# Optimization experiments

Measured on AMD Instinct MI355X. Metric: run time of the kernel, lower is better.

The kernel has to match this reference:

```python
import jax, jax.numpy as jnp
import numpy as np

B, C, D_IN, D_H, D_QK = 64, 512, 1024, 1024, 512
EPS = 1e-5


def setup_inputs() -> dict:
    key = jax.random.key(0)
    ks = jax.random.split(key, 24)
    din2 = D_IN + D_H  # concat([x, h]) feature dim
    s_qk = 1.0 / np.sqrt(din2)
    inp = {
        "x": jax.random.normal(ks[0], (B, C, D_IN), jnp.float32),
        "h": jax.random.normal(ks[1], (B, C, D_H), jnp.float32),
    }
    i = 2
    for g in ("r", "z", "n"):
        inp[f"Wq_{g}"] = jax.random.normal(ks[i], (din2, D_QK), jnp.float32) * s_qk; i += 1
        inp[f"bq_{g}"] = jnp.zeros((D_QK,), jnp.float32)
        inp[f"Wk_{g}"] = jax.random.normal(ks[i], (din2, D_QK), jnp.float32) * s_qk; i += 1
        inp[f"bk_{g}"] = jnp.zeros((D_QK,), jnp.float32)
        inp[f"Wv_{g}"] = jax.random.normal(ks[i], (din2, D_H), jnp.float32) * s_qk; i += 1
        inp[f"bv_{g}"] = jnp.zeros((D_H,), jnp.float32)
    inp["gamma"] = jnp.ones((D_H,), jnp.float32)
    inp["beta"] = jnp.zeros((D_H,), jnp.float32)
    return inp


def _self_attention(xin, Wq, bq, Wk, bk, Wv, bv):
    # xin: (B, C, 2D) ; attention over channel axis C
    Q = xin @ Wq + bq            # (B, C, d_qk)
    K = xin @ Wk + bk            # (B, C, d_qk)
    V = xin @ Wv + bv            # (B, C, d_h)
    scale = 1.0 / jnp.sqrt(jnp.asarray(Q.shape[-1], jnp.float32))
    scores = jnp.einsum("bcd,bed->bce", Q, K) * scale   # (B, C, C)
    attn = jax.nn.softmax(scores, axis=-1)
    return jnp.einsum("bce,bed->bcd", attn, V)          # (B, C, d_h)


def reference(x, h,
              Wq_r, bq_r, Wk_r, bk_r, Wv_r, bv_r,
              Wq_z, bq_z, Wk_z, bk_z, Wv_z, bv_z,
              Wq_n, bq_n, Wk_n, bk_n, Wv_n, bv_n,
              gamma, beta):
    xh = jnp.concatenate([x, h], axis=2)
    r = _self_attention(xh, Wq_r, bq_r, Wk_r, bk_r, Wv_r, bv_r)
    z = _self_attention(xh, Wq_z, bq_z, Wk_z, bk_z, Wv_z, bv_z)
    reset = jax.nn.sigmoid(r)
    update = jax.nn.sigmoid(z)
    xhr = jnp.concatenate([x, h * reset], axis=2)
    n = _self_attention(xhr, Wq_n, bq_n, Wk_n, bk_n, Wv_n, bv_n)
    new_state = (1.0 - update) * h + update * jnp.tanh(n)
    # LayerNorm over last dim
    mu = jnp.mean(new_state, axis=-1, keepdims=True)
    var = jnp.var(new_state, axis=-1, keepdims=True)
    return (new_state - mu) * jax.lax.rsqrt(var + EPS) * gamma + beta
```

## Files before the change

kernel.cpp:

```cpp
#include <hip/hip_runtime.h>
#include <math.h>

typedef __attribute__((ext_vector_type(8))) short short8;
typedef __attribute__((ext_vector_type(4))) float f32x4;

#define EPI_BF16   0
#define EPI_SCORES 1
#define EPI_R      2
#define EPI_Z      3
#define EPI_N      4

__device__ __forceinline__ unsigned short f2bf(float f) {
    unsigned int u = __float_as_uint(f);
    u += 0x7fffu + ((u >> 16) & 1u);
    return (unsigned short)(u >> 16);
}
__device__ __forceinline__ float bf2f(unsigned short s) {
    return __uint_as_float(((unsigned int)s) << 16);
}

struct alignas(8) us4 { unsigned short a, b, c, d; };

#define GLD_LDS16(gp, lp) \
    __builtin_amdgcn_global_load_lds((const __attribute__((address_space(1))) unsigned int*)(gp), \
                                     (__attribute__((address_space(3))) unsigned int*)(lp), 16, 0, 0)

__device__ __forceinline__ void BARF() {
    asm volatile("" ::: "memory");
    __builtin_amdgcn_s_barrier();
    asm volatile("" ::: "memory");
}
#define LGKM0 asm volatile("s_waitcnt lgkmcnt(0)" ::: "memory")

template<int EPI, int SWZ>
__global__ void __launch_bounds__(512, 2)
gemm256(const unsigned short* __restrict__ A, long long sAb, int lda,
        const unsigned short* __restrict__ Bt, long long sBb, int ldb,
        const float* __restrict__ bias,
        void* __restrict__ C, long long sCb, int ldc,
        int K, float scale,
        const float* __restrict__ hptr,
        const unsigned short* __restrict__ updptr)
{
    extern __shared__ char smem[];

    const int z = blockIdx.z;
    A  += (size_t)z * (size_t)sAb;
    Bt += (size_t)z * (size_t)sBb;

    int bx, by;
    if (SWZ) {
        const int bid = blockIdx.y * 8 + blockIdx.x;
        const int xcd = bid & 7, i = bid >> 3;
        bx = i & 7;
        by = (xcd << 4) | (i >> 3);
    } else {
        bx = blockIdx.x; by = blockIdx.y;
    }
    const int m0 = by * 256;
    const int n0 = bx * 256;

    const int tid = threadIdx.x;
    const int w  = tid >> 6;
    const int l  = tid & 63;
    const int wr = w >> 2;
    const int wc = w & 3;
    const int lr = l & 15;
    const int lg = l >> 4;
    const int rs = (lr & 7) << 4;

    const int srw = l >> 3;
    const int scb = ((l & 7) << 4) ^ (srw << 4);
    const int ldsw = w << 10;

    const long long ldab = (long long)lda * 2;
    const long long ldbb = (long long)ldb * 2;

    f32x4 acc[2][4][4] = {};
    short8 a[4][2], b[4][2];

#define STAGE_A(kt, buf) { \
    const char* g_ = (const char*)A + (size_t)(m0 + w*8 + srw) * ldab + (size_t)(kt)*2 + scb; \
    char* d_ = smem + (buf)*65536 + ldsw; \
    _Pragma("unroll") \
    for (int j = 0; j < 4; ++j) \
        GLD_LDS16(g_ + (size_t)(j*64) * ldab, d_ + j*8192); }

#define STAGE_B(kt, buf) { \
    const char* g_ = (const char*)Bt + (size_t)(n0 + w*8 + srw) * ldbb + (size_t)(kt)*2 + scb; \
    char* d_ = smem + (buf)*65536 + 32768 + ldsw; \
    _Pragma("unroll") \
    for (int j = 0; j < 4; ++j) \
        GLD_LDS16(g_ + (size_t)(j*64) * ldbb, d_ + j*8192); }

#define LDA8(MH, buf) { \
    const char* Ab_ = smem + (buf)*65536; \
    _Pragma("unroll") \
    for (int mf = 0; mf < 4; ++mf) { \
        const int row_ = wr*128 + (MH)*64 + mf*16 + lr; \
        _Pragma("unroll") \
        for (int kk = 0; kk < 2; ++kk) \
            a[mf][kk] = *(const short8*)(Ab_ + row_*128 + ((kk*64 + lg*16) ^ rs)); } }

#define LDB4(BH, buf) { \
    const char* Bb_ = smem + (buf)*65536 + 32768; \
    _Pragma("unroll") \
    for (int nf = 0; nf < 2; ++nf) { \
        const int row_ = wc*64 + (BH)*32 + nf*16 + lr; \
        _Pragma("unroll") \
        for (int kk = 0; kk < 2; ++kk) \
            b[(BH)*2+nf][kk] = *(const short8*)(Bb_ + row_*128 + ((kk*64 + lg*16) ^ rs)); } }

#define MMA16(MH, BH) { \
    __builtin_amdgcn_s_setprio(1); \
    _Pragma("unroll") \
    for (int kk = 0; kk < 2; ++kk) \
    _Pragma("unroll") \
    for (int mf = 0; mf < 4; ++mf) \
    _Pragma("unroll") \
    for (int nf = 0; nf < 2; ++nf) \
        acc[MH][mf][(BH)*2+nf] = __builtin_amdgcn_mfma_f32_16x16x32_bf16( \
            a[mf][kk], b[(BH)*2+nf][kk], acc[MH][mf][(BH)*2+nf], 0, 0, 0); \
    __builtin_amdgcn_s_setprio(0); }

    STAGE_A(0, 0); STAGE_B(0, 0);
    STAGE_A(64, 1); STAGE_B(64, 1);
    asm volatile("s_waitcnt vmcnt(8)" ::: "memory");
    BARF();

    const int NT = K >> 6;
    for (int t = 0; t < NT; ++t) {
        const int p = t & 1;
        LDA8(0, p); LDB4(0, p);
        BARF(); LGKM0;
        MMA16(0, 0);
        BARF();
        LDB4(1, p);
        BARF(); LGKM0;
        MMA16(0, 1);
        BARF();
        LDA8(1, p);
        BARF(); LGKM0;
        MMA16(1, 1);
        BARF();
        if (t + 2 < NT) {
            STAGE_A((t + 2) * 64, p); STAGE_B((t + 2) * 64, p);
            asm volatile("s_waitcnt vmcnt(8)" ::: "memory");
        } else {
            asm volatile("s_waitcnt vmcnt(0)" ::: "memory");
        }
        BARF();
        MMA16(1, 0);
        BARF();
    }

    const int Mb = gridDim.y << 8;
    const size_t zc = (size_t)z * (size_t)sCb;
    #pragma unroll
    for (int mh = 0; mh < 2; ++mh) {
        #pragma unroll
        for (int mf = 0; mf < 4; ++mf) {
            #pragma unroll
            for (int nf = 0; nf < 4; ++nf) {
                const int col = n0 + wc * 64 + nf * 16 + lr;
                const float bval = (EPI == EPI_BF16) ? bias[col] : 0.0f;
                #pragma unroll
                for (int r = 0; r < 4; ++r) {
                    const int row = m0 + wr * 128 + mh * 64 + mf * 16 + lg * 4 + r;
                    float v = acc[mh][mf][nf][r] + bval;
                    if (EPI == EPI_BF16) {
                        ((unsigned short*)C)[zc + (size_t)row * ldc + col] = f2bf(v);
                    } else if (EPI == EPI_SCORES) {
                        ((float*)C)[zc + (size_t)row * ldc + col] = v * scale;
                    } else if (EPI == EPI_R) {
                        const size_t flat = (size_t)z * Mb + row;
                        const float hh = hptr[flat * 1024 + col];
                        const float sg = 1.0f / (1.0f + __expf(-v));
                        ((unsigned short*)C)[flat * 2048 + 1024 + col] = f2bf(hh * sg);
                    } else if (EPI == EPI_Z) {
                        const size_t flat = (size_t)z * Mb + row;
                        const float sg = 1.0f / (1.0f + __expf(-v));
                        ((unsigned short*)C)[flat * 1024 + col] = f2bf(sg);
                    } else {
                        const size_t flat = (size_t)z * Mb + row;
                        const float u  = bf2f(updptr[flat * 1024 + col]);
                        const float hh = hptr[flat * 1024 + col];
                        ((float*)C)[flat * 1024 + col] = (1.0f - u) * hh + u * tanhf(v);
                    }
                }
            }
        }
    }
#undef STAGE_A
#undef STAGE_B
#undef LDA8
#undef LDB4
#undef MMA16
}


__global__ void __launch_bounds__(256)
prep_xh(const float* __restrict__ x, const float* __restrict__ h, unsigned short* __restrict__ xh)
{
    const size_t t = (size_t)blockIdx.x * 256 + threadIdx.x;
    const size_t f = t * 4;
    const size_t row = f >> 10, col = f & 1023;
    const float4 vx = *(const float4*)(x + f);
    const float4 vh = *(const float4*)(h + f);
    us4 ox = { f2bf(vx.x), f2bf(vx.y), f2bf(vx.z), f2bf(vx.w) };
    us4 oh = { f2bf(vh.x), f2bf(vh.y), f2bf(vh.z), f2bf(vh.w) };
    *(us4*)(xh + row * 2048 + col)        = ox;
    *(us4*)(xh + row * 2048 + 1024 + col) = oh;
}

__global__ void __launch_bounds__(256)
transpose_w(const float* __restrict__ W, unsigned short* __restrict__ WT, int N)
{
    __shared__ float t[32][33];
    const int k0 = blockIdx.y * 32, n0 = blockIdx.x * 32;
    const int tx = threadIdx.x & 31, ty = threadIdx.x >> 5;
    #pragma unroll
    for (int i = 0; i < 4; ++i)
        t[ty + i * 8][tx] = W[(size_t)(k0 + ty + i * 8) * N + n0 + tx];
    __syncthreads();
    #pragma unroll
    for (int i = 0; i < 4; ++i)
        WT[(size_t)(n0 + ty + i * 8) * 2048 + k0 + tx] = f2bf(t[tx][ty + i * 8]);
}

__global__ void __launch_bounds__(256)
transpose_v(const unsigned short* __restrict__ V, unsigned short* __restrict__ Vt)
{
    __shared__ unsigned short t[32][34];
    const int z = blockIdx.z;
    const unsigned short* in = V + (size_t)z * 512 * 2048;
    unsigned short* outp = Vt + (size_t)z * 1024 * 512;
    const int c0 = blockIdx.x * 32, r0 = blockIdx.y * 32;
    const int tx = threadIdx.x & 31, ty = threadIdx.x >> 5;
    #pragma unroll
    for (int i = 0; i < 4; ++i)
        t[ty + i * 8][tx] = in[(size_t)(r0 + ty + i * 8) * 2048 + c0 + tx];
    __syncthreads();
    #pragma unroll
    for (int i = 0; i < 4; ++i)
        outp[(size_t)(c0 + ty + i * 8) * 512 + r0 + tx] = t[tx][ty + i * 8];
}

__global__ void __launch_bounds__(256)
softmax512(const float* __restrict__ S, unsigned short* __restrict__ P)
{
    const int row = blockIdx.x * 4 + (threadIdx.x >> 6);
    const int l = threadIdx.x & 63;
    const float* s = S + (size_t)row * 512;
    const float4 v0 = ((const float4*)s)[l];
    const float4 v1 = ((const float4*)s)[64 + l];
    float m = fmaxf(fmaxf(fmaxf(v0.x, v0.y), fmaxf(v0.z, v0.w)),
                    fmaxf(fmaxf(v1.x, v1.y), fmaxf(v1.z, v1.w)));
    #pragma unroll
    for (int d = 32; d; d >>= 1) m = fmaxf(m, __shfl_xor(m, d));
    float e0 = __expf(v0.x - m), e1 = __expf(v0.y - m), e2 = __expf(v0.z - m), e3 = __expf(v0.w - m);
    float e4 = __expf(v1.x - m), e5 = __expf(v1.y - m), e6 = __expf(v1.z - m), e7 = __expf(v1.w - m);
    float sum = e0 + e1 + e2 + e3 + e4 + e5 + e6 + e7;
    #pragma unroll
    for (int d = 32; d; d >>= 1) sum += __shfl_xor(sum, d);
    const float inv = 1.0f / sum;
    unsigned short* p = P + (size_t)row * 512;
    us4 aa = { f2bf(e0 * inv), f2bf(e1 * inv), f2bf(e2 * inv), f2bf(e3 * inv) };
    us4 bb = { f2bf(e4 * inv), f2bf(e5 * inv), f2bf(e6 * inv), f2bf(e7 * inv) };
    ((us4*)p)[l] = aa;
    ((us4*)p)[64 + l] = bb;
}

__global__ void __launch_bounds__(256)
layernorm1024(float* __restrict__ Y, const float* __restrict__ gamma, const float* __restrict__ beta)
{
    const int row = blockIdx.x * 4 + (threadIdx.x >> 6);
    const int l = threadIdx.x & 63;
    float* p = Y + (size_t)row * 1024;
    float4 v[4];
    float s = 0.0f, s2 = 0.0f;
    #pragma unroll
    for (int i = 0; i < 4; ++i) {
        v[i] = ((const float4*)p)[i * 64 + l];
        s  += v[i].x + v[i].y + v[i].z + v[i].w;
        s2 += v[i].x * v[i].x + v[i].y * v[i].y + v[i].z * v[i].z + v[i].w * v[i].w;
    }
    #pragma unroll
    for (int d = 32; d; d >>= 1) { s += __shfl_xor(s, d); s2 += __shfl_xor(s2, d); }
    const float mu = s * (1.0f / 1024.0f);
    const float var = s2 * (1.0f / 1024.0f) - mu * mu;
    const float inv = rsqrtf(var + 1e-5f);
    #pragma unroll
    for (int i = 0; i < 4; ++i) {
        const float4 gv = ((const float4*)gamma)[i * 64 + l];
        const float4 bv = ((const float4*)beta)[i * 64 + l];
        float4 o;
        o.x = (v[i].x - mu) * inv * gv.x + bv.x;
        o.y = (v[i].y - mu) * inv * gv.y + bv.y;
        o.z = (v[i].z - mu) * inv * gv.z + bv.z;
        o.w = (v[i].w - mu) * inv * gv.w + bv.w;
        ((float4*)p)[i * 64 + l] = o;
    }
}

__global__ void __launch_bounds__(256)
concat_bias(const float* __restrict__ a, const float* __restrict__ b,
            const float* __restrict__ c, float* __restrict__ o)
{
    const int i = blockIdx.x * 256 + threadIdx.x;
    o[i] = (i < 512) ? a[i] : (i < 1024) ? b[i - 512] : c[i - 1024];
}

extern "C" void kernel_launch(void* const* d_in, const int* in_sizes, int n_in,
                              void* d_out, int out_size, void* d_ws, size_t ws_size,
                              hipStream_t stream)
{
    (void)in_sizes; (void)n_in; (void)out_size; (void)ws_size;

    const float* x = (const float*)d_in[0];
    const float* h = (const float*)d_in[1];
    const float* Wf[9]; const float* bia[9];
    for (int g = 0; g < 3; ++g)
        for (int j = 0; j < 3; ++j) {
            Wf[g * 3 + j]  = (const float*)d_in[2 + g * 6 + j * 2];
            bia[g * 3 + j] = (const float*)d_in[2 + g * 6 + j * 2 + 1];
        }
    const float* gamma = (const float*)d_in[20];
    const float* beta  = (const float*)d_in[21];
    float* out = (float*)d_out;

    const int LDS_BYTES = 131072;
    hipFuncSetAttribute((const void*)gemm256<EPI_BF16, 1>,   hipFuncAttributeMaxDynamicSharedMemorySize, LDS_BYTES);
    hipFuncSetAttribute((const void*)gemm256<EPI_SCORES, 0>, hipFuncAttributeMaxDynamicSharedMemorySize, LDS_BYTES);
    hipFuncSetAttribute((const void*)gemm256<EPI_R, 0>,      hipFuncAttributeMaxDynamicSharedMemorySize, LDS_BYTES);
    hipFuncSetAttribute((const void*)gemm256<EPI_Z, 0>,      hipFuncAttributeMaxDynamicSharedMemorySize, LDS_BYTES);
    hipFuncSetAttribute((const void*)gemm256<EPI_N, 0>,      hipFuncAttributeMaxDynamicSharedMemorySize, LDS_BYTES);

    char* ws = (char*)d_ws;
    size_t off = 0;
    auto alloc = [&](size_t bytes) -> void* {
        void* p = ws + off; off += (bytes + 255) & ~(size_t)255; return p;
    };
    unsigned short* xh  = (unsigned short*)alloc((size_t)32768 * 2048 * 2);
    unsigned short* WT  = (unsigned short*)alloc((size_t)12582912 * 2);
    unsigned short* QKV = (unsigned short*)alloc((size_t)32768 * 2048 * 2);
    unsigned short* Vt  = (unsigned short*)alloc((size_t)32768 * 1024 * 2);
    float*          Sc  = (float*)alloc((size_t)64 * 512 * 512 * 4);
    unsigned short* Pb  = (unsigned short*)alloc((size_t)64 * 512 * 512 * 2);
    unsigned short* upd = (unsigned short*)alloc((size_t)32768 * 1024 * 2);
    float*          bct = (float*)alloc((size_t)3 * 2048 * 4);

    size_t wtoff[9];
    {
        size_t o = 0;
        for (int g = 0; g < 3; ++g) {
            wtoff[g * 3 + 0] = o; o += (size_t)512 * 2048;
            wtoff[g * 3 + 1] = o; o += (size_t)512 * 2048;
            wtoff[g * 3 + 2] = o; o += (size_t)1024 * 2048;
        }
    }

    prep_xh<<<32768, 256, 0, stream>>>(x, h, xh);
    for (int i = 0; i < 9; ++i) {
        const int N = (i % 3 == 2) ? 1024 : 512;
        transpose_w<<<dim3(N / 32, 64, 1), 256, 0, stream>>>(Wf[i], WT + wtoff[i], N);
    }
    for (int g = 0; g < 3; ++g)
        concat_bias<<<8, 256, 0, stream>>>(bia[g * 3 + 0], bia[g * 3 + 1], bia[g * 3 + 2], bct + g * 2048);

    const float scscale = 0.044194173824159216f;

    auto gate = [&](int g, int epi) {
        const unsigned short* wT = WT + wtoff[g * 3 + 0];
        gemm256<EPI_BF16, 1><<<dim3(8, 128, 1), 512, LDS_BYTES, stream>>>(
            xh, 0, 2048, wT, 0, 2048, bct + g * 2048, QKV, 0, 2048, 2048, 0.0f, nullptr, nullptr);
        transpose_v<<<dim3(32, 16, 64), 256, 0, stream>>>(QKV + 1024, Vt);
        gemm256<EPI_SCORES, 0><<<dim3(2, 2, 64), 512, LDS_BYTES, stream>>>(
            QKV, 1048576, 2048, QKV + 512, 1048576, 2048, nullptr,
            Sc, 262144, 512, 512, scscale, nullptr, nullptr);
        softmax512<<<8192, 256, 0, stream>>>(Sc, Pb);
        if (epi == EPI_Z)
            gemm256<EPI_Z, 0><<<dim3(4, 2, 64), 512, LDS_BYTES, stream>>>(
                Pb, 262144, 512, Vt, 524288, 512, nullptr, upd, 0, 1024, 512, 0.0f, nullptr, nullptr);
        else if (epi == EPI_R)
            gemm256<EPI_R, 0><<<dim3(4, 2, 64), 512, LDS_BYTES, stream>>>(
                Pb, 262144, 512, Vt, 524288, 512, nullptr, xh, 0, 2048, 512, 0.0f, h, nullptr);
        else
            gemm256<EPI_N, 0><<<dim3(4, 2, 64), 512, LDS_BYTES, stream>>>(
                Pb, 262144, 512, Vt, 524288, 512, nullptr, out, 0, 1024, 512, 0.0f, h, upd);
    };

    gate(1, EPI_Z);
    gate(0, EPI_R);
    gate(2, EPI_N);
    layernorm1024<<<8192, 256, 0, stream>>>(out, gamma, beta);
}
```

Measured before the change: 1.575 ms.

## Restructure GEMM main loop into half-tile staged pipeline with fewer barriers

Splits each 256-row A/B LDS tile into two 128-row halves and interleaves the global-to-LDS loads of individual halves with the MFMA phases. The loop is unrolled over two k-steps with a peeled tail. It uses vmcnt(4) waits and drops the extra barriers between fragment reads and MFMAs, so loads should overlap better with compute. Each wave now holds all 8 A fragments, which raises register pressure, and the finer-grained reuse of LDS regions depends on the barrier ordering being correct.

```diff
diff --git a/kernel.cpp b/kernel.cpp
--- a/kernel.cpp
+++ b/kernel.cpp
@@ -25,12 +25,11 @@
     __builtin_amdgcn_global_load_lds((const __attribute__((address_space(1))) unsigned int*)(gp), \
                                      (__attribute__((address_space(3))) unsigned int*)(lp), 16, 0, 0)
 
-__device__ __forceinline__ void BARF() {
-    asm volatile("" ::: "memory");
-    __builtin_amdgcn_s_barrier();
-    asm volatile("" ::: "memory");
-}
-#define LGKM0 asm volatile("s_waitcnt lgkmcnt(0)" ::: "memory")
+#define BAR    __builtin_amdgcn_s_barrier()
+#define LGKM0  do { asm volatile("s_waitcnt lgkmcnt(0)" ::: "memory"); \
+                    __builtin_amdgcn_sched_barrier(0); } while (0)
+#define VMC4   asm volatile("s_waitcnt vmcnt(4)" ::: "memory")
+#define VMC0   asm volatile("s_waitcnt vmcnt(0)" ::: "memory")
 
 template<int EPI, int SWZ>
 __global__ void __launch_bounds__(512, 2)
@@ -71,42 +70,37 @@
 
     const int srw = l >> 3;
     const int scb = ((l & 7) << 4) ^ (srw << 4);
-    const int ldsw = w << 10;
 
     const long long ldab = (long long)lda * 2;
     const long long ldbb = (long long)ldb * 2;
 
     f32x4 acc[2][4][4] = {};
-    short8 a[4][2], b[4][2];
-
-#define STAGE_A(kt, buf) { \
-    const char* g_ = (const char*)A + (size_t)(m0 + w*8 + srw) * ldab + (size_t)(kt)*2 + scb; \
-    char* d_ = smem + (buf)*65536 + ldsw; \
-    _Pragma("unroll") \
-    for (int j = 0; j < 4; ++j) \
-        GLD_LDS16(g_ + (size_t)(j*64) * ldab, d_ + j*8192); }
-
-#define STAGE_B(kt, buf) { \
-    const char* g_ = (const char*)Bt + (size_t)(n0 + w*8 + srw) * ldbb + (size_t)(kt)*2 + scb; \
-    char* d_ = smem + (buf)*65536 + 32768 + ldsw; \
-    _Pragma("unroll") \
-    for (int j = 0; j < 4; ++j) \
-        GLD_LDS16(g_ + (size_t)(j*64) * ldbb, d_ + j*8192); }
+    short8 a[8][2], b[4][2];
+
+#define AR(buf, half) (smem + (buf)*65536 + (half)*16384)
+#define BR(buf, half) (smem + (buf)*65536 + 32768 + (half)*16384)
+
+#define STAGE_H(gbase, ldbytes, r0abs, kt, region) { \
+    _Pragma("unroll") \
+    for (int j = 0; j < 2; ++j) { \
+        const char* g_ = (const char*)(gbase) + \
+            (size_t)((r0abs) + j*64 + w*8 + srw) * (ldbytes) + (size_t)(kt)*2 + scb; \
+        GLD_LDS16(g_, (region) + j*8192 + (w<<10)); } }
 
 #define LDA8(MH, buf) { \
-    const char* Ab_ = smem + (buf)*65536; \
+    const char* Ab_ = AR(buf, wr); \
     _Pragma("unroll") \
     for (int mf = 0; mf < 4; ++mf) { \
-        const int row_ = wr*128 + (MH)*64 + mf*16 + lr; \
+        const int row_ = (MH)*64 + mf*16 + lr; \
         _Pragma("unroll") \
         for (int kk = 0; kk < 2; ++kk) \
-            a[mf][kk] = *(const short8*)(Ab_ + row_*128 + ((kk*64 + lg*16) ^ rs)); } }
+            a[(MH)*4+mf][kk] = *(const short8*)(Ab_ + row_*128 + ((kk*64 + lg*16) ^ rs)); } }
 
 #define LDB4(BH, buf) { \
-    const char* Bb_ = smem + (buf)*65536 + 32768; \
+    const char* Bb_ = BR(buf, wc >> 1); \
     _Pragma("unroll") \
     for (int nf = 0; nf < 2; ++nf) { \
-        const int row_ = wc*64 + (BH)*32 + nf*16 + lr; \
+        const int row_ = (wc&1)*64 + (BH)*32 + nf*16 + lr; \
         _Pragma("unroll") \
         for (int kk = 0; kk < 2; ++kk) \
             b[(BH)*2+nf][kk] = *(const short8*)(Bb_ + row_*128 + ((kk*64 + lg*16) ^ rs)); } }
@@ -120,38 +114,64 @@
     _Pragma("unroll") \
     for (int nf = 0; nf < 2; ++nf) \
         acc[MH][mf][(BH)*2+nf] = __builtin_amdgcn_mfma_f32_16x16x32_bf16( \
-            a[mf][kk], b[(BH)*2+nf][kk], acc[MH][mf][(BH)*2+nf], 0, 0, 0); \
+            a[(MH)*4+mf][kk], b[(BH)*2+nf][kk], acc[MH][mf][(BH)*2+nf], 0, 0, 0); \
     __builtin_amdgcn_s_setprio(0); }
 
-    STAGE_A(0, 0); STAGE_B(0, 0);
-    STAGE_A(64, 1); STAGE_B(64, 1);
-    asm volatile("s_waitcnt vmcnt(8)" ::: "memory");
-    BARF();
-
-    const int NT = K >> 6;
-    for (int t = 0; t < NT; ++t) {
-        const int p = t & 1;
-        LDA8(0, p); LDB4(0, p);
-        BARF(); LGKM0;
-        MMA16(0, 0);
-        BARF();
-        LDB4(1, p);
-        BARF(); LGKM0;
-        MMA16(0, 1);
-        BARF();
-        LDA8(1, p);
-        BARF(); LGKM0;
+    STAGE_H(A,  ldab, m0 + 0,   0,  AR(0,0));
+    STAGE_H(A,  ldab, m0 + 128, 0,  AR(0,1));
+    STAGE_H(Bt, ldbb, n0 + 0,   0,  BR(0,0));
+    STAGE_H(Bt, ldbb, n0 + 128, 0,  BR(0,1));
+    STAGE_H(A,  ldab, m0 + 0,   64, AR(1,0));
+    STAGE_H(A,  ldab, m0 + 128, 64, AR(1,1));
+
+    const int NIT = K >> 7;
+    for (int it = 0; it < NIT - 1; ++it) {
+        const int kt0 = it << 7;
+        VMC4; BAR;
+        STAGE_H(Bt, ldbb, n0 + 0,   kt0 + 64,  BR(1,0));
+        LDA8(0, 0); LDB4(0, 0);
+        LGKM0; MMA16(0, 0);
+        BAR;
+        STAGE_H(Bt, ldbb, n0 + 128, kt0 + 64,  BR(1,1));
+        LDA8(1, 0); LDB4(1, 0);
+        LGKM0; MMA16(0, 1);
+        BAR;
+        STAGE_H(A,  ldab, m0 + 0,   kt0 + 128, AR(0,0));
         MMA16(1, 1);
-        BARF();
-        if (t + 2 < NT) {
-            STAGE_A((t + 2) * 64, p); STAGE_B((t + 2) * 64, p);
-            asm volatile("s_waitcnt vmcnt(8)" ::: "memory");
-        } else {
-            asm volatile("s_waitcnt vmcnt(0)" ::: "memory");
-        }
-        BARF();
+        BAR;
+        STAGE_H(A,  ldab, m0 + 128, kt0 + 128, AR(0,1));
         MMA16(1, 0);
-        BARF();
+        VMC4; BAR;
+        STAGE_H(Bt, ldbb, n0 + 0,   kt0 + 128, BR(0,0));
+        LDA8(0, 1); LDB4(0, 1);
+        LGKM0; MMA16(0, 0);
+        BAR;
+        STAGE_H(Bt, ldbb, n0 + 128, kt0 + 128, BR(0,1));
+        LDA8(1, 1); LDB4(1, 1);
+        LGKM0; MMA16(0, 1);
+        BAR;
+        STAGE_H(A,  ldab, m0 + 0,   kt0 + 192, AR(1,0));
+        MMA16(1, 1);
+        BAR;
+        STAGE_H(A,  ldab, m0 + 128, kt0 + 192, AR(1,1));
+        MMA16(1, 0);
+    }
+    {
+        const int kt0 = (NIT - 1) << 7;
+        VMC4; BAR;
+        STAGE_H(Bt, ldbb, n0 + 0,   kt0 + 64, BR(1,0));
+        LDA8(0, 0); LDB4(0, 0); LGKM0; MMA16(0, 0);
+        BAR;
+        STAGE_H(Bt, ldbb, n0 + 128, kt0 + 64, BR(1,1));
+        LDA8(1, 0); LDB4(1, 0); LGKM0; MMA16(0, 1);
+        BAR; MMA16(1, 1);
+        BAR; MMA16(1, 0);
+        VMC0; BAR;
+        LDA8(0, 1); LDB4(0, 1); LGKM0; MMA16(0, 0);
+        BAR;
+        LDA8(1, 1); LDB4(1, 1); LGKM0; MMA16(0, 1);
+        BAR; MMA16(1, 1);
+        BAR; MMA16(1, 0);
     }
 
     const int Mb = gridDim.y << 8;
@@ -191,8 +211,9 @@
             }
         }
     }
-#undef STAGE_A
-#undef STAGE_B
+#undef AR
+#undef BR
+#undef STAGE_H
 #undef LDA8
 #undef LDB4
 #undef MMA16
```

Result: slower. 1.978 ms (+25.6%).

## Interleave split global-to-LDS staging with MFMA phases and drop barriers

Applied to the files above, without the earlier changes.

Prefetching in the GEMM main loop is split into quarter-tile global_load_lds chunks, issued between the LDS fragment reads and the MFMA phases instead of all at once before the last phase. B is now prefetched one tile ahead into the alternate buffer, while A stays two tiles ahead in the current buffer. Several barriers and the explicit lgkmcnt(0) waits are removed, and the vmcnt waits are retuned to the new load order. The aim is to overlap global loads with matrix work and cut synchronisation stalls. The cost is a more fragile ordering of LDS reads against in-flight overwrites.

```diff
diff --git a/kernel.cpp b/kernel.cpp
--- a/kernel.cpp
+++ b/kernel.cpp
@@ -25,12 +25,10 @@
     __builtin_amdgcn_global_load_lds((const __attribute__((address_space(1))) unsigned int*)(gp), \
                                      (__attribute__((address_space(3))) unsigned int*)(lp), 16, 0, 0)
 
-__device__ __forceinline__ void BARF() {
-    asm volatile("" ::: "memory");
-    __builtin_amdgcn_s_barrier();
-    asm volatile("" ::: "memory");
-}
-#define LGKM0 asm volatile("s_waitcnt lgkmcnt(0)" ::: "memory")
+#define BAR   do { asm volatile("" ::: "memory"); __builtin_amdgcn_s_barrier(); \
+                   asm volatile("" ::: "memory"); } while (0)
+#define VMC4  asm volatile("s_waitcnt vmcnt(4)" ::: "memory")
+#define VMC0  asm volatile("s_waitcnt vmcnt(0)" ::: "memory")
 
 template<int EPI, int SWZ>
 __global__ void __launch_bounds__(512, 2)
@@ -71,7 +69,6 @@
 
     const int srw = l >> 3;
     const int scb = ((l & 7) << 4) ^ (srw << 4);
-    const int ldsw = w << 10;
 
     const long long ldab = (long long)lda * 2;
     const long long ldbb = (long long)ldb * 2;
@@ -79,22 +76,25 @@
     f32x4 acc[2][4][4] = {};
     short8 a[4][2], b[4][2];
 
-#define STAGE_A(kt, buf) { \
-    const char* g_ = (const char*)A + (size_t)(m0 + w*8 + srw) * ldab + (size_t)(kt)*2 + scb; \
-    char* d_ = smem + (buf)*65536 + ldsw; \
-    _Pragma("unroll") \
-    for (int j = 0; j < 4; ++j) \
-        GLD_LDS16(g_ + (size_t)(j*64) * ldab, d_ + j*8192); }
-
-#define STAGE_B(kt, buf) { \
-    const char* g_ = (const char*)Bt + (size_t)(n0 + w*8 + srw) * ldbb + (size_t)(kt)*2 + scb; \
-    char* d_ = smem + (buf)*65536 + 32768 + ldsw; \
-    _Pragma("unroll") \
-    for (int j = 0; j < 4; ++j) \
-        GLD_LDS16(g_ + (size_t)(j*64) * ldbb, d_ + j*8192); }
+#define STAGE1(gbase, ldbytes, grow0, ldsoff) { \
+    const char* g_ = (const char*)(gbase) + \
+        (size_t)((grow0) + w*8 + srw) * (ldbytes) + scb; \
+    GLD_LDS16(g_, smem + (ldsoff) + (w << 10)); }
+
+#define AOFF(buf) ((buf)*65536)
+#define BOFF(buf) ((buf)*65536 + 32768)
+
+#define STAGE_A0(kt, buf) { STAGE1(A, ldab, m0 + 0   + 0*0, AOFF(buf) + 0);      \
+                            STAGE1(A + (size_t)(kt)*0, ldab, m0 + 128, AOFF(buf) + 16384); } (void)0
+#define STAGE_B0(kt, buf) { STAGE1(Bt, ldbb, n0 + 0,   BOFF(buf) + 0);      \
+                            STAGE1(Bt, ldbb, n0 + 128, BOFF(buf) + 16384); } (void)0
+#define STAGE_A1(kt, buf) { STAGE1(A, ldab, m0 + 64,  AOFF(buf) + 8192);  \
+                            STAGE1(A, ldab, m0 + 192, AOFF(buf) + 24576); } (void)0
+#define STAGE_B1(kt, buf) { STAGE1(Bt, ldbb, n0 + 64,  BOFF(buf) + 8192);  \
+                            STAGE1(Bt, ldbb, n0 + 192, BOFF(buf) + 24576); } (void)0
 
 #define LDA8(MH, buf) { \
-    const char* Ab_ = smem + (buf)*65536; \
+    const char* Ab_ = smem + AOFF(buf); \
     _Pragma("unroll") \
     for (int mf = 0; mf < 4; ++mf) { \
         const int row_ = wr*128 + (MH)*64 + mf*16 + lr; \
@@ -103,7 +103,7 @@
             a[mf][kk] = *(const short8*)(Ab_ + row_*128 + ((kk*64 + lg*16) ^ rs)); } }
 
 #define LDB4(BH, buf) { \
-    const char* Bb_ = smem + (buf)*65536 + 32768; \
+    const char* Bb_ = smem + BOFF(buf); \
     _Pragma("unroll") \
     for (int nf = 0; nf < 2; ++nf) { \
         const int row_ = wc*64 + (BH)*32 + nf*16 + lr; \
@@ -123,35 +123,56 @@
             a[mf][kk], b[(BH)*2+nf][kk], acc[MH][mf][(BH)*2+nf], 0, 0, 0); \
     __builtin_amdgcn_s_setprio(0); }
 
-    STAGE_A(0, 0); STAGE_B(0, 0);
-    STAGE_A(64, 1); STAGE_B(64, 1);
-    asm volatile("s_waitcnt vmcnt(8)" ::: "memory");
-    BARF();
+    {
+        const unsigned short* A0p = A;           const unsigned short* B0p = Bt;
+        (void)A0p; (void)B0p;
+        { const long long kb = 0;
+          STAGE1(A  + (kb>>1), ldab, m0 + 0,   AOFF(0) + 0);
+          STAGE1(A  + (kb>>1), ldab, m0 + 128, AOFF(0) + 16384);
+          STAGE1(A  + (kb>>1), ldab, m0 + 64,  AOFF(0) + 8192);
+          STAGE1(A  + (kb>>1), ldab, m0 + 192, AOFF(0) + 24576);
+          STAGE1(Bt + (kb>>1), ldbb, n0 + 0,   BOFF(0) + 0);
+          STAGE1(Bt + (kb>>1), ldbb, n0 + 128, BOFF(0) + 16384);
+          STAGE1(Bt + (kb>>1), ldbb, n0 + 64,  BOFF(0) + 8192);
+          STAGE1(Bt + (kb>>1), ldbb, n0 + 192, BOFF(0) + 24576); }
+        { const long long kb = 128;
+          STAGE1(A  + (kb>>1), ldab, m0 + 0,   AOFF(1) + 0);
+          STAGE1(A  + (kb>>1), ldab, m0 + 128, AOFF(1) + 16384);
+          STAGE1(A  + (kb>>1), ldab, m0 + 64,  AOFF(1) + 8192);
+          STAGE1(A  + (kb>>1), ldab, m0 + 192, AOFF(1) + 24576); }
+        VMC4;
+        BAR;
+    }
 
     const int NT = K >> 6;
     for (int t = 0; t < NT; ++t) {
-        const int p = t & 1;
+        const int p = t & 1, q = p ^ 1;
+        const unsigned short* An = A  + (size_t)(t + 2) * 64;
+        const unsigned short* Bn = Bt + (size_t)(t + 1) * 64;
+        const bool sB = (t + 1 < NT), sA = (t + 2 < NT);
+
         LDA8(0, p); LDB4(0, p);
-        BARF(); LGKM0;
+        if (sB) { STAGE1(Bn, ldbb, n0 + 0,   BOFF(q) + 0);
+                  STAGE1(Bn, ldbb, n0 + 128, BOFF(q) + 16384); }
+        BAR;
         MMA16(0, 0);
-        BARF();
         LDB4(1, p);
-        BARF(); LGKM0;
+        if (sB) { STAGE1(Bn, ldbb, n0 + 64,  BOFF(q) + 8192);
+                  STAGE1(Bn, ldbb, n0 + 192, BOFF(q) + 24576); }
+        BAR;
         MMA16(0, 1);
-        BARF();
         LDA8(1, p);
-        BARF(); LGKM0;
+        if (sA) { STAGE1(An, ldab, m0 + 0,   AOFF(p) + 0);
+                  STAGE1(An, ldab, m0 + 128, AOFF(p) + 16384); }
+        BAR;
         MMA16(1, 1);
-        BARF();
-        if (t + 2 < NT) {
-            STAGE_A((t + 2) * 64, p); STAGE_B((t + 2) * 64, p);
-            asm volatile("s_waitcnt vmcnt(8)" ::: "memory");
-        } else {
-            asm volatile("s_waitcnt vmcnt(0)" ::: "memory");
-        }
-        BARF();
+        BAR;
+        if (sA) { STAGE1(An, ldab, m0 + 64,  AOFF(p) + 8192);
+                  STAGE1(An, ldab, m0 + 192, AOFF(p) + 24576);
+                  VMC4; }
+        else if (sB) { VMC0; }
+        BAR;
         MMA16(1, 0);
-        BARF();
     }
 
     const int Mb = gridDim.y << 8;
@@ -191,8 +212,13 @@
             }
         }
     }
-#undef STAGE_A
-#undef STAGE_B
+#undef STAGE1
+#undef AOFF
+#undef BOFF
+#undef STAGE_A0
+#undef STAGE_A1
+#undef STAGE_B0
+#undef STAGE_B1
 #undef LDA8
 #undef LDB4
 #undef MMA16
```

Result: faster. 1.407 ms (-10.6%).
